# Performance work log

Measured on AMD Instinct MI355X. Metric: run time of the kernel, lower is better.

The kernel has to match this reference:

```python
import jax, jax.numpy as jnp
import numpy as np

NUM_LAYERS = 4
INPUT_DIM = 512
BATCH = 16384


def setup_inputs() -> dict:
    key = jax.random.key(0)
    kx, kw, kb = jax.random.split(key, 3)
    x = jax.random.normal(kx, (BATCH, INPUT_DIM), dtype=jnp.float32)
    # PyTorch nn.Linear init: U(-1/sqrt(fan_in), 1/sqrt(fan_in))
    bound = 1.0 / np.sqrt(INPUT_DIM)
    W = jax.random.uniform(kw, (NUM_LAYERS, INPUT_DIM, INPUT_DIM), jnp.float32, -bound, bound)
    b = jax.random.uniform(kb, (NUM_LAYERS, INPUT_DIM), jnp.float32, -bound, bound)
    return {"x": x, "W": W, "b": b}


def reference(x, W, b):
    # x: [B, D]; W: [L, D, D] (torch Linear weight, so y = x @ W_i.T + b_i)
    x_list = [x]
    for i in range(NUM_LAYERS):
        x_ = x_list[-1]
        # sequentially accumulate dot-product residuals against all prior activations
        for x_pre in x_list[:-1]:
            s = jnp.sum(x_ * x_pre, axis=-1, keepdims=True)  # [B, 1]
            x_ = x_ + s
        y = jnp.einsum("bd,ed->be", x_, W[i]) + b[i]  # Linear: x_ @ W_i.T + b_i
        x_list.append(y)
    out = jnp.concatenate(x_list[1:], axis=-1)  # [B, L*D]
    return out
```

## Files before the change

### kernel.cpp

```cpp
#include <hip/hip_runtime.h>
#include <stdint.h>


#define BROWS 16384
#define DIM 512
#define NL 4
#define OUTSTRIDE (NL * DIM)

#define BM 64
#define BK 32
#define SEG (DIM / BK)
#define NSTEP (NL * SEG)

typedef unsigned short ushort_t;
typedef __attribute__((ext_vector_type(8))) short bf16x8;
typedef __attribute__((ext_vector_type(4))) float f32x4;

__device__ inline ushort_t f32_to_bf16(float f) {
    union { float f; uint32_t u; } v; v.f = f;
    uint32_t u = v.u;
    uint32_t r = (u + 0x7fffu + ((u >> 16) & 1u)) >> 16;
    return (ushort_t)r;
}

__device__ inline float bf16_lo(uint32_t p) {
    union { uint32_t u; float f; } v; v.u = p << 16; return v.f;
}
__device__ inline float bf16_hi(uint32_t p) {
    union { uint32_t u; float f; } v; v.u = p & 0xffff0000u; return v.f;
}

__device__ inline float wave_reduce_sum(float v) {
    #pragma unroll
    for (int off = 32; off > 0; off >>= 1) v += __shfl_down(v, off, 64);
    return v;
}

__global__ __launch_bounds__(256) void prep_kernel(
    const float* __restrict__ W, ushort_t* __restrict__ Wb,
    float* __restrict__ wsum)
{
    int row = blockIdx.x;
    int t = threadIdx.x;
    const float* wp = W + (size_t)row * DIM;
    float f0 = wp[2 * t], f1 = wp[2 * t + 1];
    ushort_t* wbp = Wb + (size_t)row * DIM;
    wbp[2 * t]     = f32_to_bf16(f0);
    wbp[2 * t + 1] = f32_to_bf16(f1);
    __shared__ float red[4];
    int wave = t >> 6, lane = t & 63;
    float r = wave_reduce_sum(f0 + f1);
    if (lane == 0) red[wave] = r;
    __syncthreads();
    if (t == 0) wsum[row] = red[0] + red[1] + red[2] + red[3];
}

__global__ __launch_bounds__(512, 1) void cross_kernel(
    const float* __restrict__ x0,
    const ushort_t* __restrict__ Wb,
    const float* __restrict__ bias,
    const float* __restrict__ wsum,
    float* __restrict__ out)
{
    __shared__ __align__(16) ushort_t sAct[BM * DIM];
    __shared__ __align__(16) ushort_t sB[2][DIM * BK];
    __shared__ float sRed[4][4][BM];
    __shared__ float sSums[4][BM];
    __shared__ float sCn[BM];

    int tid  = threadIdx.x;
    int wave = tid >> 6;
    int lane = tid & 63;
    int wm  = wave >> 2;
    int wn4 = wave & 3;
    int q = lane >> 4;
    int rr = lane & 15;
    int nlane = lane & 15;
    int bm = blockIdx.x * BM;

    int beoff[4];
    #pragma unroll
    for (int j = 0; j < 4; ++j) {
        int brow = wave * 64 + j * 16 + (lane >> 2);
        int chunk = (lane & 3) ^ (brow & 3);
        beoff[j] = brow * DIM + chunk * 8;
    }

    auto stageB = [&](int s) {
        int cur = s & 1;
        const ushort_t* gb = Wb + (size_t)(s >> 4) * DIM * DIM + (s & 15) * BK;
        #pragma unroll
        for (int j = 0; j < 4; ++j) {
            __builtin_amdgcn_global_load_lds(
                (const __attribute__((address_space(1))) void*)(gb + beoff[j]),
                (__attribute__((address_space(3))) void*)(&sB[cur][(wave * 64 + j * 16) * BK]),
                16, 0, 0);
        }
    };

    stageB(0);

    #pragma unroll
    for (int r8 = 0; r8 < 8; ++r8) {
        int row = wave * 8 + r8;
        const float* xp = x0 + (size_t)(bm + row) * DIM + lane * 8;
        float4 a = ((const float4*)xp)[0];
        float4 b4 = ((const float4*)xp)[1];
        float f[8] = {a.x, a.y, a.z, a.w, b4.x, b4.y, b4.z, b4.w};
        bf16x8 o;
        float s = 0.f;
        #pragma unroll
        for (int i = 0; i < 8; ++i) { o[i] = (short)f32_to_bf16(f[i]); s += f[i]; }
        int kc = lane ^ (row & 7);
        *(bf16x8*)(&sAct[row * DIM + kc * 8]) = o;
        s = wave_reduce_sum(s);
        if (lane == 0) sSums[0][row] = s;
    }
    __syncthreads();

    uint32_t vk0[32], vk1[32], vk2[32];

    #pragma unroll
    for (int l = 0; l < NL; ++l) {
        f32x4 acc[2][8] = {};

        for (int t = 0; t < SEG; ++t) {
            int s = l * SEG + t;
            int cur = s & 1;
            asm volatile("s_waitcnt vmcnt(0)" ::: "memory");
            __builtin_amdgcn_s_barrier();
            if (s + 1 < NSTEP) stageB(s + 1);

            bf16x8 af[2], bfr[8];
            #pragma unroll
            for (int mi = 0; mi < 2; ++mi) {
                int arow = wm * 32 + mi * 16 + rr;
                int kc = (t * 4 + q) ^ (arow & 7);
                af[mi] = *(const bf16x8*)(&sAct[arow * DIM + kc * 8]);
            }
            int ch2 = q ^ (rr & 3);
            #pragma unroll
            for (int ni = 0; ni < 8; ++ni) {
                int erow = wn4 * 128 + ni * 16 + rr;
                bfr[ni] = *(const bf16x8*)(&sB[cur][erow * BK + ch2 * 8]);
            }
            #pragma unroll
            for (int mi = 0; mi < 2; ++mi)
                #pragma unroll
                for (int ni = 0; ni < 8; ++ni)
                    acc[mi][ni] = __builtin_amdgcn_mfma_f32_16x16x32_bf16(
                        af[mi], bfr[ni], acc[mi][ni], 0, 0, 0);
        }

        __syncthreads();

        float ws8[8], bs8[8];
        #pragma unroll
        for (int ni = 0; ni < 8; ++ni) {
            int ng = wn4 * 128 + ni * 16 + nlane;
            ws8[ni] = wsum[l * DIM + ng];
            bs8[ni] = bias[l * DIM + ng];
        }
        float cl8[8];
        #pragma unroll
        for (int mi = 0; mi < 2; ++mi)
            #pragma unroll
            for (int r = 0; r < 4; ++r)
                cl8[mi * 4 + r] = (l == 0) ? 0.f : sCn[wm * 32 + mi * 16 + q * 4 + r];

        if (l == 0) {
            #pragma unroll
            for (int mi = 0; mi < 2; ++mi)
                #pragma unroll
                for (int r = 0; r < 4; ++r) {
                    int row = wm * 32 + mi * 16 + q * 4 + r;
                    #pragma unroll
                    for (int nip = 0; nip < 4; ++nip) {
                        int kc0 = (wn4 * 16 + 4 * nip + (nlane >> 3)) ^ (row & 7);
                        int kc1 = (wn4 * 16 + 4 * nip + 2 + (nlane >> 3)) ^ (row & 7);
                        uint32_t b0 = sAct[row * DIM + kc0 * 8 + (nlane & 7)];
                        uint32_t b1 = sAct[row * DIM + kc1 * 8 + (nlane & 7)];
                        vk0[(mi * 4 + r) * 4 + nip] = b0 | (b1 << 16);
                    }
                }
        }

        #pragma unroll
        for (int mi = 0; mi < 2; ++mi)
            #pragma unroll
            for (int r = 0; r < 4; ++r) {
                int mr = mi * 4 + r;
                int row = wm * 32 + mi * 16 + q * 4 + r;
                float cc = cl8[mr];
                float vv[8];
                #pragma unroll
                for (int ni = 0; ni < 8; ++ni) {
                    vv[ni] = acc[mi][ni][r] + cc * ws8[ni] + bs8[ni];
                    int colg = wn4 * 128 + ni * 16 + nlane;
                    __builtin_nontemporal_store(
                        vv[ni], &out[(size_t)(bm + row) * OUTSTRIDE + l * DIM + colg]);
                }
                if (l < 3) {
                    float vs = 0.f, d0 = 0.f, d1 = 0.f, d2 = 0.f;
                    #pragma unroll
                    for (int ni = 0; ni < 8; ++ni) vs += vv[ni];
                    #pragma unroll
                    for (int nip = 0; nip < 4; ++nip) {
                        uint32_t p0 = vk0[mr * 4 + nip];
                        d0 += vv[2 * nip] * bf16_lo(p0) + vv[2 * nip + 1] * bf16_hi(p0);
                        if (l >= 1) {
                            uint32_t p1 = vk1[mr * 4 + nip];
                            d1 += vv[2 * nip] * bf16_lo(p1) + vv[2 * nip + 1] * bf16_hi(p1);
                        }
                        if (l >= 2) {
                            uint32_t p2 = vk2[mr * 4 + nip];
                            d2 += vv[2 * nip] * bf16_lo(p2) + vv[2 * nip + 1] * bf16_hi(p2);
                        }
                    }
                    #pragma unroll
                    for (int nip = 0; nip < 4; ++nip) {
                        ushort_t h0 = f32_to_bf16(vv[2 * nip]);
                        ushort_t h1 = f32_to_bf16(vv[2 * nip + 1]);
                        int kc0 = (wn4 * 16 + 4 * nip + (nlane >> 3)) ^ (row & 7);
                        int kc1 = (wn4 * 16 + 4 * nip + 2 + (nlane >> 3)) ^ (row & 7);
                        sAct[row * DIM + kc0 * 8 + (nlane & 7)] = h0;
                        sAct[row * DIM + kc1 * 8 + (nlane & 7)] = h1;
                        uint32_t pk = (uint32_t)h0 | ((uint32_t)h1 << 16);
                        if (l == 0) vk1[mr * 4 + nip] = pk;
                        if (l == 1) vk2[mr * 4 + nip] = pk;
                    }
                    #pragma unroll
                    for (int off = 8; off > 0; off >>= 1) {
                        vs += __shfl_xor(vs, off, 64);
                        d0 += __shfl_xor(d0, off, 64);
                        if (l >= 1) d1 += __shfl_xor(d1, off, 64);
                        if (l >= 2) d2 += __shfl_xor(d2, off, 64);
                    }
                    if (nlane == 0) {
                        sRed[0][wn4][row] = vs;
                        sRed[1][wn4][row] = d0;
                        if (l >= 1) sRed[2][wn4][row] = d1;
                        if (l >= 2) sRed[3][wn4][row] = d2;
                    }
                }
            }

        if (l < 3) {
            __syncthreads();
            if (tid < BM) {
                float vs = sRed[0][0][tid] + sRed[0][1][tid] + sRed[0][2][tid] + sRed[0][3][tid];
                float d0 = sRed[1][0][tid] + sRed[1][1][tid] + sRed[1][2][tid] + sRed[1][3][tid];
                float c = d0;
                if (l >= 1) {
                    float d1 = sRed[2][0][tid] + sRed[2][1][tid] + sRed[2][2][tid] + sRed[2][3][tid];
                    c = c + d1 + c * sSums[1][tid];
                }
                if (l >= 2) {
                    float d2 = sRed[3][0][tid] + sRed[3][1][tid] + sRed[3][2][tid] + sRed[3][3][tid];
                    c = c + d2 + c * sSums[2][tid];
                }
                sCn[tid] = c;
                sSums[l + 1][tid] = vs;
            }
            __syncthreads();
        }
    }
}

extern "C" void kernel_launch(void* const* d_in, const int* in_sizes, int n_in,
                              void* d_out, int out_size, void* d_ws, size_t ws_size,
                              hipStream_t stream) {
    (void)in_sizes; (void)n_in; (void)out_size; (void)ws_size;
    const float* x0   = (const float*)d_in[0];
    const float* W    = (const float*)d_in[1];
    const float* bias = (const float*)d_in[2];
    float* out = (float*)d_out;

    char* ws = (char*)d_ws;
    ushort_t* Wb   = (ushort_t*)ws;
    float*    wsum = (float*)(ws + 2097152);

    prep_kernel<<<NL * DIM, 256, 0, stream>>>(W, Wb, wsum);
    cross_kernel<<<BROWS / BM, 512, 0, stream>>>(x0, Wb, bias, wsum, out);
}
```

Before: 278.9 us.

## Double waves per block to 16 and read prior activations from LDS

```diff
diff --git a/kernel.cpp b/kernel.cpp
--- a/kernel.cpp
+++ b/kernel.cpp
@@ -21,6 +21,10 @@
     uint32_t u = v.u;
     uint32_t r = (u + 0x7fffu + ((u >> 16) & 1u)) >> 16;
     return (ushort_t)r;
+}
+
+__device__ inline float bf16_bits_to_f32(ushort_t u) {
+    union { uint32_t u; float f; } v; v.u = ((uint32_t)u) << 16; return v.f;
 }
 
 __device__ inline float bf16_lo(uint32_t p) {
@@ -55,7 +59,7 @@
     if (t == 0) wsum[row] = red[0] + red[1] + red[2] + red[3];
 }
 
-__global__ __launch_bounds__(512, 1) void cross_kernel(
+__global__ __launch_bounds__(1024) void cross_kernel(
     const float* __restrict__ x0,
     const ushort_t* __restrict__ Wb,
     const float* __restrict__ bias,
@@ -64,45 +68,40 @@
 {
     __shared__ __align__(16) ushort_t sAct[BM * DIM];
     __shared__ __align__(16) ushort_t sB[2][DIM * BK];
-    __shared__ float sRed[4][4][BM];
-    __shared__ float sSums[4][BM];
+    __shared__ float sRed[4][8][BM];
+    __shared__ float sSums[NL][BM];
     __shared__ float sCn[BM];
 
-    int tid  = threadIdx.x;
-    int wave = tid >> 6;
-    int lane = tid & 63;
-    int wm  = wave >> 2;
-    int wn4 = wave & 3;
-    int q = lane >> 4;
-    int rr = lane & 15;
-    int nlane = lane & 15;
-    int bm = blockIdx.x * BM;
-
-    int beoff[4];
+    const int tid  = threadIdx.x;
+    const int wave = tid >> 6;
+    const int lane = tid & 63;
+    const int wm   = wave >> 3;
+    const int wn8  = wave & 7;
+    const int q    = lane >> 4;
+    const int rr   = lane & 15;
+    const int nlane = lane & 15;
+    const int bm   = blockIdx.x * BM;
+
+    const int srow = lane >> 2;
+
+    auto stageB = [&](int s) {
+        const ushort_t* gb = Wb + (size_t)(s >> 4) * (DIM * DIM) + (s & 15) * BK;
+        #pragma unroll
+        for (int c = 0; c < 2; ++c) {
+            int r0 = wave * 32 + c * 16;
+            int grow = r0 + srow;
+            int gchunk = (lane & 3) ^ (grow & 3);
+            __builtin_amdgcn_global_load_lds(
+                (const __attribute__((address_space(1))) void*)(gb + (size_t)grow * DIM + gchunk * 8),
+                (__attribute__((address_space(3))) void*)(&sB[s & 1][r0 * BK]), 16, 0, 0);
+        }
+    };
+
+    stageB(0);
+
     #pragma unroll
-    for (int j = 0; j < 4; ++j) {
-        int brow = wave * 64 + j * 16 + (lane >> 2);
-        int chunk = (lane & 3) ^ (brow & 3);
-        beoff[j] = brow * DIM + chunk * 8;
-    }
-
-    auto stageB = [&](int s) {
-        int cur = s & 1;
-        const ushort_t* gb = Wb + (size_t)(s >> 4) * DIM * DIM + (s & 15) * BK;
-        #pragma unroll
-        for (int j = 0; j < 4; ++j) {
-            __builtin_amdgcn_global_load_lds(
-                (const __attribute__((address_space(1))) void*)(gb + beoff[j]),
-                (__attribute__((address_space(3))) void*)(&sB[cur][(wave * 64 + j * 16) * BK]),
-                16, 0, 0);
-        }
-    };
-
-    stageB(0);
-
-    #pragma unroll
-    for (int r8 = 0; r8 < 8; ++r8) {
-        int row = wave * 8 + r8;
+    for (int r4 = 0; r4 < 4; ++r4) {
+        int row = wave * 4 + r4;
         const float* xp = x0 + (size_t)(bm + row) * DIM + lane * 8;
         float4 a = ((const float4*)xp)[0];
         float4 b4 = ((const float4*)xp)[1];
@@ -111,123 +110,117 @@
         float s = 0.f;
         #pragma unroll
         for (int i = 0; i < 8; ++i) { o[i] = (short)f32_to_bf16(f[i]); s += f[i]; }
-        int kc = lane ^ (row & 7);
+        int kc = lane ^ (row & 15);
         *(bf16x8*)(&sAct[row * DIM + kc * 8]) = o;
         s = wave_reduce_sum(s);
         if (lane == 0) sSums[0][row] = s;
     }
     __syncthreads();
 
-    uint32_t vk0[32], vk1[32], vk2[32];
+    uint32_t vk0[16], vk1[16];
 
     #pragma unroll
     for (int l = 0; l < NL; ++l) {
-        f32x4 acc[2][8] = {};
+        f32x4 acc[2][4] = {};
 
         for (int t = 0; t < SEG; ++t) {
             int s = l * SEG + t;
-            int cur = s & 1;
             asm volatile("s_waitcnt vmcnt(0)" ::: "memory");
             __builtin_amdgcn_s_barrier();
             if (s + 1 < NSTEP) stageB(s + 1);
 
-            bf16x8 af[2], bfr[8];
+            bf16x8 af[2], bfr[4];
             #pragma unroll
             for (int mi = 0; mi < 2; ++mi) {
-                int arow = wm * 32 + mi * 16 + rr;
-                int kc = (t * 4 + q) ^ (arow & 7);
-                af[mi] = *(const bf16x8*)(&sAct[arow * DIM + kc * 8]);
-            }
-            int ch2 = q ^ (rr & 3);
-            #pragma unroll
-            for (int ni = 0; ni < 8; ++ni) {
-                int erow = wn4 * 128 + ni * 16 + rr;
-                bfr[ni] = *(const bf16x8*)(&sB[cur][erow * BK + ch2 * 8]);
+                int row = wm * 32 + mi * 16 + rr;
+                int kc = (4 * t + q) ^ (row & 15);
+                af[mi] = *(const bf16x8*)(&sAct[row * DIM + kc * 8]);
+            }
+            #pragma unroll
+            for (int ni = 0; ni < 4; ++ni) {
+                int erow = wn8 * 64 + ni * 16 + rr;
+                int bc = q ^ (erow & 3);
+                bfr[ni] = *(const bf16x8*)(&sB[s & 1][erow * BK + bc * 8]);
             }
             #pragma unroll
             for (int mi = 0; mi < 2; ++mi)
                 #pragma unroll
-                for (int ni = 0; ni < 8; ++ni)
+                for (int ni = 0; ni < 4; ++ni)
                     acc[mi][ni] = __builtin_amdgcn_mfma_f32_16x16x32_bf16(
                         af[mi], bfr[ni], acc[mi][ni], 0, 0, 0);
         }
 
         __syncthreads();
 
-        float ws8[8], bs8[8];
-        #pragma unroll
-        for (int ni = 0; ni < 8; ++ni) {
-            int ng = wn4 * 128 + ni * 16 + nlane;
-            ws8[ni] = wsum[l * DIM + ng];
-            bs8[ni] = bias[l * DIM + ng];
-        }
-        float cl8[8];
+        float ws4[4], bs4[4];
+        #pragma unroll
+        for (int ni = 0; ni < 4; ++ni) {
+            int ng = wn8 * 64 + ni * 16 + nlane;
+            ws4[ni] = wsum[l * DIM + ng];
+            bs4[ni] = bias[l * DIM + ng];
+        }
+
         #pragma unroll
         for (int mi = 0; mi < 2; ++mi)
             #pragma unroll
-            for (int r = 0; r < 4; ++r)
-                cl8[mi * 4 + r] = (l == 0) ? 0.f : sCn[wm * 32 + mi * 16 + q * 4 + r];
-
-        if (l == 0) {
-            #pragma unroll
-            for (int mi = 0; mi < 2; ++mi)
+            for (int r = 0; r < 4; ++r) {
+                const int mr = mi * 4 + r;
+                const int row = wm * 32 + mi * 16 + q * 4 + r;
+                float cc = (l == 0) ? 0.f : sCn[row];
+                float vv[4];
                 #pragma unroll
-                for (int r = 0; r < 4; ++r) {
-                    int row = wm * 32 + mi * 16 + q * 4 + r;
-                    #pragma unroll
-                    for (int nip = 0; nip < 4; ++nip) {
-                        int kc0 = (wn4 * 16 + 4 * nip + (nlane >> 3)) ^ (row & 7);
-                        int kc1 = (wn4 * 16 + 4 * nip + 2 + (nlane >> 3)) ^ (row & 7);
-                        uint32_t b0 = sAct[row * DIM + kc0 * 8 + (nlane & 7)];
-                        uint32_t b1 = sAct[row * DIM + kc1 * 8 + (nlane & 7)];
-                        vk0[(mi * 4 + r) * 4 + nip] = b0 | (b1 << 16);
-                    }
-                }
-        }
-
-        #pragma unroll
-        for (int mi = 0; mi < 2; ++mi)
-            #pragma unroll
-            for (int r = 0; r < 4; ++r) {
-                int mr = mi * 4 + r;
-                int row = wm * 32 + mi * 16 + q * 4 + r;
-                float cc = cl8[mr];
-                float vv[8];
-                #pragma unroll
-                for (int ni = 0; ni < 8; ++ni) {
-                    vv[ni] = acc[mi][ni][r] + cc * ws8[ni] + bs8[ni];
-                    int colg = wn4 * 128 + ni * 16 + nlane;
-                    __builtin_nontemporal_store(
-                        vv[ni], &out[(size_t)(bm + row) * OUTSTRIDE + l * DIM + colg]);
+                for (int ni = 0; ni < 4; ++ni) {
+                    vv[ni] = acc[mi][ni][r] + cc * ws4[ni] + bs4[ni];
+                    int colg = wn8 * 64 + ni * 16 + nlane;
+                    out[(size_t)(bm + row) * OUTSTRIDE + l * DIM + colg] = vv[ni];
                 }
                 if (l < 3) {
-                    float vs = 0.f, d0 = 0.f, d1 = 0.f, d2 = 0.f;
-                    #pragma unroll
-                    for (int ni = 0; ni < 8; ++ni) vs += vv[ni];
-                    #pragma unroll
-                    for (int nip = 0; nip < 4; ++nip) {
-                        uint32_t p0 = vk0[mr * 4 + nip];
-                        d0 += vv[2 * nip] * bf16_lo(p0) + vv[2 * nip + 1] * bf16_hi(p0);
-                        if (l >= 1) {
-                            uint32_t p1 = vk1[mr * 4 + nip];
-                            d1 += vv[2 * nip] * bf16_lo(p1) + vv[2 * nip + 1] * bf16_hi(p1);
+                    ushort_t xl[4];
+                    #pragma unroll
+                    for (int ni = 0; ni < 4; ++ni) {
+                        int cg = wn8 * 8 + ni * 2 + (nlane >> 3);
+                        int kc = cg ^ (row & 15);
+                        xl[ni] = sAct[row * DIM + kc * 8 + (nlane & 7)];
+                    }
+                    float vs = 0.f, dc = 0.f;
+                    #pragma unroll
+                    for (int ni = 0; ni < 4; ++ni) {
+                        vs += vv[ni];
+                        dc += vv[ni] * bf16_bits_to_f32(xl[ni]);
+                    }
+                    float d0 = 0.f, d1 = 0.f, d2 = 0.f;
+                    if (l == 0) {
+                        d0 = dc;
+                        #pragma unroll
+                        for (int nip = 0; nip < 2; ++nip)
+                            vk0[mr * 2 + nip] =
+                                (uint32_t)xl[2 * nip] | ((uint32_t)xl[2 * nip + 1] << 16);
+                    } else {
+                        #pragma unroll
+                        for (int nip = 0; nip < 2; ++nip) {
+                            uint32_t p = vk0[mr * 2 + nip];
+                            d0 += vv[2 * nip] * bf16_lo(p) + vv[2 * nip + 1] * bf16_hi(p);
                         }
-                        if (l >= 2) {
-                            uint32_t p2 = vk2[mr * 4 + nip];
-                            d2 += vv[2 * nip] * bf16_lo(p2) + vv[2 * nip + 1] * bf16_hi(p2);
+                        if (l == 1) {
+                            d1 = dc;
+                            #pragma unroll
+                            for (int nip = 0; nip < 2; ++nip)
+                                vk1[mr * 2 + nip] =
+                                    (uint32_t)xl[2 * nip] | ((uint32_t)xl[2 * nip + 1] << 16);
+                        } else {
+                            #pragma unroll
+                            for (int nip = 0; nip < 2; ++nip) {
+                                uint32_t p = vk1[mr * 2 + nip];
+                                d1 += vv[2 * nip] * bf16_lo(p) + vv[2 * nip + 1] * bf16_hi(p);
+                            }
+                            d2 = dc;
                         }
                     }
                     #pragma unroll
-                    for (int nip = 0; nip < 4; ++nip) {
-                        ushort_t h0 = f32_to_bf16(vv[2 * nip]);
-                        ushort_t h1 = f32_to_bf16(vv[2 * nip + 1]);
-                        int kc0 = (wn4 * 16 + 4 * nip + (nlane >> 3)) ^ (row & 7);
-                        int kc1 = (wn4 * 16 + 4 * nip + 2 + (nlane >> 3)) ^ (row & 7);
-                        sAct[row * DIM + kc0 * 8 + (nlane & 7)] = h0;
-                        sAct[row * DIM + kc1 * 8 + (nlane & 7)] = h1;
-                        uint32_t pk = (uint32_t)h0 | ((uint32_t)h1 << 16);
-                        if (l == 0) vk1[mr * 4 + nip] = pk;
-                        if (l == 1) vk2[mr * 4 + nip] = pk;
+                    for (int ni = 0; ni < 4; ++ni) {
+                        int cg = wn8 * 8 + ni * 2 + (nlane >> 3);
+                        int kc = cg ^ (row & 15);
+                        sAct[row * DIM + kc * 8 + (nlane & 7)] = f32_to_bf16(vv[ni]);
                     }
                     #pragma unroll
                     for (int off = 8; off > 0; off >>= 1) {
@@ -237,10 +230,10 @@
                         if (l >= 2) d2 += __shfl_xor(d2, off, 64);
                     }
                     if (nlane == 0) {
-                        sRed[0][wn4][row] = vs;
-                        sRed[1][wn4][row] = d0;
-                        if (l >= 1) sRed[2][wn4][row] = d1;
-                        if (l >= 2) sRed[3][wn4][row] = d2;
+                        sRed[0][wn8][row] = vs;
+                        sRed[1][wn8][row] = d0;
+                        if (l >= 1) sRed[2][wn8][row] = d1;
+                        if (l >= 2) sRed[3][wn8][row] = d2;
                     }
                 }
             }
@@ -248,15 +241,20 @@
         if (l < 3) {
             __syncthreads();
             if (tid < BM) {
-                float vs = sRed[0][0][tid] + sRed[0][1][tid] + sRed[0][2][tid] + sRed[0][3][tid];
-                float d0 = sRed[1][0][tid] + sRed[1][1][tid] + sRed[1][2][tid] + sRed[1][3][tid];
+                float vs = 0.f, d0 = 0.f;
+                #pragma unroll
+                for (int g = 0; g < 8; ++g) { vs += sRed[0][g][tid]; d0 += sRed[1][g][tid]; }
                 float c = d0;
                 if (l >= 1) {
-                    float d1 = sRed[2][0][tid] + sRed[2][1][tid] + sRed[2][2][tid] + sRed[2][3][tid];
+                    float d1 = 0.f;
+                    #pragma unroll
+                    for (int g = 0; g < 8; ++g) d1 += sRed[2][g][tid];
                     c = c + d1 + c * sSums[1][tid];
                 }
                 if (l >= 2) {
-                    float d2 = sRed[3][0][tid] + sRed[3][1][tid] + sRed[3][2][tid] + sRed[3][3][tid];
+                    float d2 = 0.f;
+                    #pragma unroll
+                    for (int g = 0; g < 8; ++g) d2 += sRed[3][g][tid];
                     c = c + d2 + c * sSums[2][tid];
                 }
                 sCn[tid] = c;
@@ -281,5 +279,5 @@
     float*    wsum = (float*)(ws + 2097152);
 
     prep_kernel<<<NL * DIM, 256, 0, stream>>>(W, Wb, wsum);
-    cross_kernel<<<BROWS / BM, 512, 0, stream>>>(x0, Wb, bias, wsum, out);
-}
+    cross_kernel<<<BROWS / BM, 1024, 0, stream>>>(x0, Wb, bias, wsum, out);
+}
```

Result: faster. 265.5 us (-4.8%).
